# Kernel optimization log

Hardware: AMD Instinct MI355X
Metric: run time of the kernel (lower is better)

Reference implementation:

```python
import jax, jax.numpy as jnp
import numpy as np

N = 100000
IN_C = 128
OUT_C = 128
E = 1600000


def setup_inputs() -> dict:
    key = jax.random.key(0)
    k1, k2, k3, k4 = jax.random.split(key, 4)
    x = jax.random.normal(k1, (N, IN_C), dtype=jnp.float32)
    edge_index = jax.random.randint(k2, (2, E), 0, N, dtype=jnp.int64)
    # GCNConv params: linear weight (stored [in, out] for x @ W) and bias [out]
    W = jax.random.normal(k3, (IN_C, OUT_C), dtype=jnp.float32) / np.sqrt(IN_C)
    b = jax.random.normal(k4, (OUT_C,), dtype=jnp.float32) * 0.01
    return {"x": x, "edge_index": edge_index, "W": W, "b": b}


def reference(x, edge_index, W, b):
    n = x.shape[0]
    # add self loops (PyG GCNConv default add_self_loops=True)
    loop = jnp.arange(n, dtype=edge_index.dtype)
    src = jnp.concatenate([edge_index[0], loop])  # message sources
    dst = jnp.concatenate([edge_index[1], loop])  # aggregation targets
    # symmetric normalization: deg over targets (edge weight 1, incl. self loops)
    deg = jax.ops.segment_sum(jnp.ones_like(dst, dtype=x.dtype), dst, num_segments=n)
    dinv = jnp.where(deg > 0, jax.lax.rsqrt(deg), 0.0)
    norm = dinv[src] * dinv[dst]  # [E+N]
    # linear transform then gather-scale-scatter aggregation
    h = x @ W  # [N, out]
    msgs = h[src] * norm[:, None]  # [E+N, out] -- dominant memory traffic
    out = jax.ops.segment_sum(msgs, dst, num_segments=n)
    return out + b
```

## Files before the change

### kernel.cpp

```cpp
#include <hip/hip_runtime.h>


#define SCAN_T 256
#define SCAN_E 1024
#define WPB 4
#define CAP 1536
#define SC_T 8192

typedef __attribute__((ext_vector_type(8))) short short8;
typedef __attribute__((ext_vector_type(4))) float f32x4;

__device__ __forceinline__ unsigned short f2bf(float f) {
  unsigned int u = __float_as_uint(f);
  u += 0x7FFFu + ((u >> 16) & 1u);
  return (unsigned short)(u >> 16);
}
__device__ __forceinline__ float bf_lo(unsigned int u) { return __uint_as_float(u << 16); }
__device__ __forceinline__ float bf_hi(unsigned int u) { return __uint_as_float(u & 0xFFFF0000u); }


__global__ void k_zero(int* __restrict__ p, int m) {
  int i = blockIdx.x * blockDim.x + threadIdx.x;
  if (i < m) p[i] = 0;
}

__global__ void __launch_bounds__(512) k_scatter(
    const int* __restrict__ ei, int* __restrict__ bcursor,
    int* __restrict__ pairs, int E, int B) {
  __shared__ int hist[2048];
  int t = threadIdx.x;
  for (int b = t; b < B; b += 512) hist[b] = 0;
  __syncthreads();
  int e0 = blockIdx.x * SC_T;
  int eend = min(e0 + SC_T, E);
  for (int e = e0 + t * 4; e < eend; e += 2048) {
    if (e + 3 < eend) {
      int4 d = *(const int4*)(ei + E + e);
      atomicAdd(&hist[((unsigned)d.x) >> 6], 1);
      atomicAdd(&hist[((unsigned)d.y) >> 6], 1);
      atomicAdd(&hist[((unsigned)d.z) >> 6], 1);
      atomicAdd(&hist[((unsigned)d.w) >> 6], 1);
    } else {
      for (int q = e; q < eend; ++q) atomicAdd(&hist[((unsigned)ei[E + q]) >> 6], 1);
    }
  }
  __syncthreads();
  for (int b = t; b < B; b += 512) {
    int c = hist[b];
    hist[b] = c ? atomicAdd(&bcursor[b], c) : 0;
  }
  __syncthreads();
  for (int e = e0 + t * 4; e < eend; e += 2048) {
    if (e + 3 < eend) {
      int4 s = *(const int4*)(ei + e);
      int4 d = *(const int4*)(ei + E + e);
      int b0 = ((unsigned)d.x) >> 6; int p0 = atomicAdd(&hist[b0], 1);
      if (p0 < CAP) pairs[(size_t)b0 * CAP + p0] = ((d.x & 63) << 17) | s.x;
      int b1 = ((unsigned)d.y) >> 6; int p1 = atomicAdd(&hist[b1], 1);
      if (p1 < CAP) pairs[(size_t)b1 * CAP + p1] = ((d.y & 63) << 17) | s.y;
      int b2 = ((unsigned)d.z) >> 6; int p2 = atomicAdd(&hist[b2], 1);
      if (p2 < CAP) pairs[(size_t)b2 * CAP + p2] = ((d.z & 63) << 17) | s.z;
      int b3 = ((unsigned)d.w) >> 6; int p3 = atomicAdd(&hist[b3], 1);
      if (p3 < CAP) pairs[(size_t)b3 * CAP + p3] = ((d.w & 63) << 17) | s.w;
    } else {
      for (int q = e; q < eend; ++q) {
        int dst = ei[E + q], src = ei[q];
        int b0 = ((unsigned)dst) >> 6; int p0 = atomicAdd(&hist[b0], 1);
        if (p0 < CAP) pairs[(size_t)b0 * CAP + p0] = ((dst & 63) << 17) | src;
      }
    }
  }
}

__global__ void __launch_bounds__(256) k_sort_gemm(
    int* __restrict__ pairs, const int* __restrict__ bcursor,
    int* __restrict__ onc, float* __restrict__ dinv,
    const float* __restrict__ x, const float* __restrict__ W,
    unsigned short* __restrict__ h, int n) {
  __shared__ alignas(16) unsigned short Wt[128][136];
  __shared__ int pb[CAP];
  __shared__ int sorted[CAP];
  __shared__ int hist[64], base_[64], cur[64];
  __shared__ float dloc[64];
  int t = threadIdx.x;
  int b = blockIdx.x;
  if (t < 64) { hist[t] = 0; cur[t] = 0; }
  int cnt = min(bcursor[b], CAP);
  int* gp = pairs + (size_t)b * CAP;
  for (int i = t; i < cnt; i += 256) pb[i] = gp[i];
#pragma unroll
  for (int p = 0; p < 16; ++p) {
    int task = p * 256 + t;
    int kg = task >> 7, nn = task & 127;
    float w0 = W[(kg * 4 + 0) * 128 + nn];
    float w1 = W[(kg * 4 + 1) * 128 + nn];
    float w2 = W[(kg * 4 + 2) * 128 + nn];
    float w3 = W[(kg * 4 + 3) * 128 + nn];
    ushort4 u;
    u.x = f2bf(w0); u.y = f2bf(w1); u.z = f2bf(w2); u.w = f2bf(w3);
    *(ushort4*)&Wt[nn][kg * 4] = u;
  }
  __syncthreads();
  for (int i = t; i < cnt; i += 256) atomicAdd(&hist[pb[i] >> 17], 1);
  __syncthreads();
  if (t < 64) {
    int v = hist[t];
    int incl = v;
#pragma unroll
    for (int d = 1; d < 64; d <<= 1) {
      int u = __shfl_up(incl, d, 64);
      if (t >= d) incl += u;
    }
    base_[t] = incl - v;
    float di = rsqrtf((float)v + 1.0f);
    dloc[t] = di;
    int node = b * 64 + t;
    if (node < n) {
      onc[node] = ((incl - v) << 16) | v;
      dinv[node] = di;
    }
  }
  __syncthreads();
  for (int i = t; i < cnt; i += 256) {
    int p = pb[i];
    int d = p >> 17;
    int pos = base_[d] + atomicAdd(&cur[d], 1);
    sorted[pos] = p & 0x1FFFF;
  }
  __syncthreads();
  for (int i = t; i < cnt; i += 256) gp[i] = sorted[i];

  int w = t >> 6, lane = t & 63;
  int q = lane >> 4, m = lane & 15;
  int r0 = b * 64 + w * 16;
  f32x4 acc[8];
#pragma unroll
  for (int nt = 0; nt < 8; ++nt) acc[nt] = (f32x4){0.f, 0.f, 0.f, 0.f};
  float dscale[4];
#pragma unroll
  for (int rg = 0; rg < 4; ++rg) dscale[rg] = dloc[w * 16 + q * 4 + rg];
#pragma unroll
  for (int ks = 0; ks < 4; ++ks) {
    int row = r0 + m;
    row = row < n ? row : n - 1;
    const float* xp = x + (size_t)row * 128 + ks * 32 + q * 8;
    float4 a0 = *(const float4*)xp;
    float4 a1 = *(const float4*)(xp + 4);
    short8 af;
    af[0] = (short)f2bf(a0.x); af[1] = (short)f2bf(a0.y);
    af[2] = (short)f2bf(a0.z); af[3] = (short)f2bf(a0.w);
    af[4] = (short)f2bf(a1.x); af[5] = (short)f2bf(a1.y);
    af[6] = (short)f2bf(a1.z); af[7] = (short)f2bf(a1.w);
#pragma unroll
    for (int nt = 0; nt < 8; ++nt) {
      short8 bf = *(const short8*)&Wt[nt * 16 + m][ks * 32 + q * 8];
      acc[nt] = __builtin_amdgcn_mfma_f32_16x16x32_bf16(af, bf, acc[nt], 0, 0, 0);
    }
  }
#pragma unroll
  for (int nt = 0; nt < 8; ++nt)
#pragma unroll
    for (int rg = 0; rg < 4; ++rg) {
      int r = r0 + q * 4 + rg;
      if (r < n) h[(size_t)r * 128 + nt * 16 + m] = f2bf(acc[nt][rg] * dscale[rg]);
    }
}

__global__ void __launch_bounds__(256) k_agg_bias(
    const unsigned int* __restrict__ h2, const float* __restrict__ dinv,
    const int* __restrict__ onc, const int* __restrict__ pairs,
    const float* __restrict__ bias, float* __restrict__ out, int n) {
  int node = blockIdx.x * WPB + (threadIdx.x >> 6);
  int lane = threadIdx.x & 63;
  if (node >= n) return;
  unsigned int sp = h2[(size_t)node * 64 + lane];
  float ax = bf_lo(sp), ay = bf_hi(sp);
  int v = onc[node];
  int s = (node >> 6) * CAP + (v >> 16);
  int end = s + (v & 0xFFFF);
  const int* __restrict__ csr = pairs;
  for (; s + 8 <= end; s += 8) {
    int i0 = csr[s + 0], i1 = csr[s + 1], i2 = csr[s + 2], i3 = csr[s + 3];
    int i4 = csr[s + 4], i5 = csr[s + 5], i6 = csr[s + 6], i7 = csr[s + 7];
    unsigned int u0 = h2[(size_t)i0 * 64 + lane];
    unsigned int u1 = h2[(size_t)i1 * 64 + lane];
    unsigned int u2 = h2[(size_t)i2 * 64 + lane];
    unsigned int u3 = h2[(size_t)i3 * 64 + lane];
    unsigned int u4 = h2[(size_t)i4 * 64 + lane];
    unsigned int u5 = h2[(size_t)i5 * 64 + lane];
    unsigned int u6 = h2[(size_t)i6 * 64 + lane];
    unsigned int u7 = h2[(size_t)i7 * 64 + lane];
    ax += (bf_lo(u0) + bf_lo(u1)) + (bf_lo(u2) + bf_lo(u3)) +
          (bf_lo(u4) + bf_lo(u5)) + (bf_lo(u6) + bf_lo(u7));
    ay += (bf_hi(u0) + bf_hi(u1)) + (bf_hi(u2) + bf_hi(u3)) +
          (bf_hi(u4) + bf_hi(u5)) + (bf_hi(u6) + bf_hi(u7));
  }
  for (; s < end; ++s) {
    unsigned int u = h2[(size_t)csr[s] * 64 + lane];
    ax += bf_lo(u); ay += bf_hi(u);
  }
  float di = dinv[node];
  float2 bb = ((const float2*)bias)[lane];
  float2 r;
  r.x = fmaf(ax, di, bb.x);
  r.y = fmaf(ay, di, bb.y);
  ((float2*)out)[(size_t)node * 64 + lane] = r;
}


__global__ void k_init(int* __restrict__ cnt, int n) {
  int i = blockIdx.x * blockDim.x + threadIdx.x;
  if (i < n) cnt[i] = 0;
}

__global__ void k_count4(const int* __restrict__ ei, int* __restrict__ cnt, int E) {
  int i = blockIdx.x * blockDim.x + threadIdx.x;
  int e = i * 4;
  if (e + 3 < E) {
    int4 d = *(const int4*)(ei + E + e);
    atomicAdd(&cnt[d.x], 1); atomicAdd(&cnt[d.y], 1);
    atomicAdd(&cnt[d.z], 1); atomicAdd(&cnt[d.w], 1);
  } else {
    for (; e < E; ++e) atomicAdd(&cnt[ei[E + e]], 1);
  }
}

__global__ void k_scan_local(const int* __restrict__ cnt, int* __restrict__ offs,
                             int* __restrict__ bsums, int n) {
  __shared__ int sh[SCAN_T];
  int t = threadIdx.x;
  int base = blockIdx.x * SCAN_E + t * 4;
  int v0 = 0, v1 = 0, v2 = 0, v3 = 0;
  if (base + 0 < n) v0 = cnt[base + 0];
  if (base + 1 < n) v1 = cnt[base + 1];
  if (base + 2 < n) v2 = cnt[base + 2];
  if (base + 3 < n) v3 = cnt[base + 3];
  int sum = v0 + v1 + v2 + v3;
  sh[t] = sum;
  __syncthreads();
  for (int d = 1; d < SCAN_T; d <<= 1) {
    int xv = (t >= d) ? sh[t - d] : 0;
    __syncthreads();
    sh[t] += xv;
    __syncthreads();
  }
  int run = sh[t] - sum;
  if (base + 0 < n) offs[base + 0] = run; run += v0;
  if (base + 1 < n) offs[base + 1] = run; run += v1;
  if (base + 2 < n) offs[base + 2] = run; run += v2;
  if (base + 3 < n) offs[base + 3] = run;
  if (t == SCAN_T - 1) bsums[blockIdx.x] = sh[t];
}

__global__ void k_scan_bsums(int* __restrict__ bsums, int nb) {
  __shared__ int sh[SCAN_T];
  int t = threadIdx.x;
  int v = (t < nb) ? bsums[t] : 0;
  sh[t] = v;
  __syncthreads();
  for (int d = 1; d < SCAN_T; d <<= 1) {
    int xv = (t >= d) ? sh[t - d] : 0;
    __syncthreads();
    sh[t] += xv;
    __syncthreads();
  }
  if (t < nb) bsums[t] = sh[t] - v;
}

__global__ void k_scan_finish(int* __restrict__ offs, const int* __restrict__ bsums,
                              const int* __restrict__ cnt, int* __restrict__ offs2,
                              float* __restrict__ dinv, int n) {
  int i = blockIdx.x * blockDim.x + threadIdx.x;
  if (i < n) {
    int o = offs[i] + bsums[i / SCAN_E];
    offs[i] = o;
    offs2[i] = o;
    dinv[i] = rsqrtf((float)cnt[i] + 1.0f);
  }
}

__global__ void k_fill4(const int* __restrict__ ei, int* __restrict__ offs2,
                        int* __restrict__ csr, int E) {
  int i = blockIdx.x * blockDim.x + threadIdx.x;
  int e = i * 4;
  if (e + 3 < E) {
    int4 s = *(const int4*)(ei + e);
    int4 d = *(const int4*)(ei + E + e);
    csr[atomicAdd(&offs2[d.x], 1)] = s.x;
    csr[atomicAdd(&offs2[d.y], 1)] = s.y;
    csr[atomicAdd(&offs2[d.z], 1)] = s.z;
    csr[atomicAdd(&offs2[d.w], 1)] = s.w;
  } else {
    for (; e < E; ++e) csr[atomicAdd(&offs2[ei[E + e]], 1)] = ei[e];
  }
}

__global__ void __launch_bounds__(256) k_gemm_h(
    const float* __restrict__ x, const float* __restrict__ W,
    const float* __restrict__ dinv, unsigned short* __restrict__ h, int n) {
  __shared__ alignas(16) unsigned short Wt[128][136];
  int t = threadIdx.x;
#pragma unroll
  for (int p = 0; p < 16; ++p) {
    int task = p * 256 + t;
    int kg = task >> 7, nn = task & 127;
    float w0 = W[(kg * 4 + 0) * 128 + nn];
    float w1 = W[(kg * 4 + 1) * 128 + nn];
    float w2 = W[(kg * 4 + 2) * 128 + nn];
    float w3 = W[(kg * 4 + 3) * 128 + nn];
    ushort4 u;
    u.x = f2bf(w0); u.y = f2bf(w1); u.z = f2bf(w2); u.w = f2bf(w3);
    *(ushort4*)&Wt[nn][kg * 4] = u;
  }
  __syncthreads();
  int w = t >> 6, lane = t & 63;
  int q = lane >> 4, m = lane & 15;
  int r0 = blockIdx.x * 64 + w * 16;
  f32x4 acc[8];
#pragma unroll
  for (int nt = 0; nt < 8; ++nt) acc[nt] = (f32x4){0.f, 0.f, 0.f, 0.f};
  float dscale[4];
#pragma unroll
  for (int rg = 0; rg < 4; ++rg) {
    int r = r0 + q * 4 + rg;
    dscale[rg] = dinv[r < n ? r : n - 1];
  }
#pragma unroll
  for (int ks = 0; ks < 4; ++ks) {
    int row = r0 + m;
    row = row < n ? row : n - 1;
    const float* xp = x + (size_t)row * 128 + ks * 32 + q * 8;
    float4 a0 = *(const float4*)xp;
    float4 a1 = *(const float4*)(xp + 4);
    short8 af;
    af[0] = (short)f2bf(a0.x); af[1] = (short)f2bf(a0.y);
    af[2] = (short)f2bf(a0.z); af[3] = (short)f2bf(a0.w);
    af[4] = (short)f2bf(a1.x); af[5] = (short)f2bf(a1.y);
    af[6] = (short)f2bf(a1.z); af[7] = (short)f2bf(a1.w);
#pragma unroll
    for (int nt = 0; nt < 8; ++nt) {
      short8 bf = *(const short8*)&Wt[nt * 16 + m][ks * 32 + q * 8];
      acc[nt] = __builtin_amdgcn_mfma_f32_16x16x32_bf16(af, bf, acc[nt], 0, 0, 0);
    }
  }
#pragma unroll
  for (int nt = 0; nt < 8; ++nt)
#pragma unroll
    for (int rg = 0; rg < 4; ++rg) {
      int r = r0 + q * 4 + rg;
      if (r < n) h[(size_t)r * 128 + nt * 16 + m] = f2bf(acc[nt][rg] * dscale[rg]);
    }
}

__global__ void __launch_bounds__(256) k_agg_bias_csr(
    const unsigned int* __restrict__ h2, const float* __restrict__ dinv,
    const int* __restrict__ offs, const int* __restrict__ cnt,
    const int* __restrict__ csr, const float* __restrict__ bias,
    float* __restrict__ out, int n) {
  int node = blockIdx.x * WPB + (threadIdx.x >> 6);
  int lane = threadIdx.x & 63;
  if (node >= n) return;
  unsigned int sp = h2[(size_t)node * 64 + lane];
  float ax = bf_lo(sp), ay = bf_hi(sp);
  int s = offs[node];
  int end = s + cnt[node];
  for (; s + 8 <= end; s += 8) {
    int i0 = csr[s + 0], i1 = csr[s + 1], i2 = csr[s + 2], i3 = csr[s + 3];
    int i4 = csr[s + 4], i5 = csr[s + 5], i6 = csr[s + 6], i7 = csr[s + 7];
    unsigned int u0 = h2[(size_t)i0 * 64 + lane];
    unsigned int u1 = h2[(size_t)i1 * 64 + lane];
    unsigned int u2 = h2[(size_t)i2 * 64 + lane];
    unsigned int u3 = h2[(size_t)i3 * 64 + lane];
    unsigned int u4 = h2[(size_t)i4 * 64 + lane];
    unsigned int u5 = h2[(size_t)i5 * 64 + lane];
    unsigned int u6 = h2[(size_t)i6 * 64 + lane];
    unsigned int u7 = h2[(size_t)i7 * 64 + lane];
    ax += (bf_lo(u0) + bf_lo(u1)) + (bf_lo(u2) + bf_lo(u3)) +
          (bf_lo(u4) + bf_lo(u5)) + (bf_lo(u6) + bf_lo(u7));
    ay += (bf_hi(u0) + bf_hi(u1)) + (bf_hi(u2) + bf_hi(u3)) +
          (bf_hi(u4) + bf_hi(u5)) + (bf_hi(u6) + bf_hi(u7));
  }
  for (; s < end; ++s) {
    unsigned int u = h2[(size_t)csr[s] * 64 + lane];
    ax += bf_lo(u); ay += bf_hi(u);
  }
  float di = dinv[node];
  float2 bb = ((const float2*)bias)[lane];
  float2 r;
  r.x = fmaf(ax, di, bb.x);
  r.y = fmaf(ay, di, bb.y);
  ((float2*)out)[(size_t)node * 64 + lane] = r;
}

extern "C" void kernel_launch(void* const* d_in, const int* in_sizes, int n_in,
                              void* d_out, int out_size, void* d_ws, size_t ws_size,
                              hipStream_t stream) {
  const float* x = (const float*)d_in[0];
  const int* ei = (const int*)d_in[1];
  const float* Wm = (const float*)d_in[2];
  const float* bias = (const float*)d_in[3];
  float* out = (float*)d_out;

  int N = in_sizes[0] / 128;
  int E = in_sizes[1] / 2;
  int NB = (N + 63) >> 6;

  size_t need_new = (size_t)N * 8 + 8192 + (size_t)NB * CAP * 4 + (size_t)N * 256;

  if (ws_size >= need_new && N <= (1 << 17) && NB <= 2048) {
    char* p = (char*)d_ws;
    float* dinv = (float*)p;       p += (size_t)N * 4;
    int* onc = (int*)p;            p += (size_t)N * 4;
    int* bcursor = (int*)p;        p += 8192;
    int* pairs = (int*)p;          p += (size_t)NB * CAP * 4;
    unsigned short* h = (unsigned short*)p;

    k_zero<<<(NB + 255) / 256, 256, 0, stream>>>(bcursor, NB);
    k_scatter<<<(E + SC_T - 1) / SC_T, 512, 0, stream>>>(ei, bcursor, pairs, E, NB);
    k_sort_gemm<<<NB, 256, 0, stream>>>(pairs, bcursor, onc, dinv, x, Wm, h, N);
    k_agg_bias<<<(N + WPB - 1) / WPB, 256, 0, stream>>>(
        (const unsigned int*)h, dinv, onc, pairs, bias, out, N);
    return;
  }

  char* p = (char*)d_ws;
  int* cnt = (int*)p;        p += (size_t)N * 4;
  int* offs = (int*)p;       p += (size_t)N * 4;
  int* offs2 = (int*)p;      p += (size_t)N * 4;
  float* dinv = (float*)p;   p += (size_t)N * 4;
  int* bsums = (int*)p;      p += 1024;
  int* csr = (int*)p;        p += (size_t)E * 4;
  unsigned short* h = (unsigned short*)p;

  int nb_n = (N + 255) / 256;
  int nb_e4 = ((E + 3) / 4 + 255) / 256;
  int nb_scan = (N + SCAN_E - 1) / SCAN_E;

  k_init<<<nb_n, 256, 0, stream>>>(cnt, N);
  k_count4<<<nb_e4, 256, 0, stream>>>(ei, cnt, E);
  k_scan_local<<<nb_scan, SCAN_T, 0, stream>>>(cnt, offs, bsums, N);
  k_scan_bsums<<<1, SCAN_T, 0, stream>>>(bsums, nb_scan);
  k_scan_finish<<<nb_n, 256, 0, stream>>>(offs, bsums, cnt, offs2, dinv, N);
  k_fill4<<<nb_e4, 256, 0, stream>>>(ei, offs2, csr, E);
  k_gemm_h<<<(N + 63) / 64, 256, 0, stream>>>(x, Wm, dinv, h, N);
  k_agg_bias_csr<<<(N + WPB - 1) / WPB, 256, 0, stream>>>(
      (const unsigned int*)h, dinv, offs, cnt, csr, bias, out, N);
}
```

Baseline: 221.2 us.

## Overlap edge scatter with GEMM in one launch, split bucket sort out

The edge bucket-scatter and the dense x@W GEMM now share one launch: the first SB blocks scatter edges and the remaining blocks run the MFMA GEMM, so the two independent phases run concurrently. The per-bucket CSR sort and degree computation move to a separate kernel. Because the GEMM no longer has the degree, h is stored unscaled, and the aggregation kernel instead loads dinv[src] per edge and applies it with an FMA. This adds one small kernel launch and an extra gathered 4-byte load per edge in the memory-bound aggregation, in exchange for hiding the scatter behind the GEMM. The scatter tile size is halved to match 256-thread blocks.

```diff
diff --git a/kernel.cpp b/kernel.cpp
--- a/kernel.cpp
+++ b/kernel.cpp
@@ -5,7 +5,7 @@
 #define SCAN_E 1024
 #define WPB 4
 #define CAP 1536
-#define SC_T 8192
+#define SC_T 4096
 
 typedef __attribute__((ext_vector_type(8))) short short8;
 typedef __attribute__((ext_vector_type(4))) float f32x4;
@@ -24,70 +24,63 @@
   if (i < m) p[i] = 0;
 }
 
-__global__ void __launch_bounds__(512) k_scatter(
+__global__ void __launch_bounds__(256) k_scatter_gemm(
     const int* __restrict__ ei, int* __restrict__ bcursor,
-    int* __restrict__ pairs, int E, int B) {
-  __shared__ int hist[2048];
-  int t = threadIdx.x;
-  for (int b = t; b < B; b += 512) hist[b] = 0;
-  __syncthreads();
-  int e0 = blockIdx.x * SC_T;
-  int eend = min(e0 + SC_T, E);
-  for (int e = e0 + t * 4; e < eend; e += 2048) {
-    if (e + 3 < eend) {
-      int4 d = *(const int4*)(ei + E + e);
-      atomicAdd(&hist[((unsigned)d.x) >> 6], 1);
-      atomicAdd(&hist[((unsigned)d.y) >> 6], 1);
-      atomicAdd(&hist[((unsigned)d.z) >> 6], 1);
-      atomicAdd(&hist[((unsigned)d.w) >> 6], 1);
-    } else {
-      for (int q = e; q < eend; ++q) atomicAdd(&hist[((unsigned)ei[E + q]) >> 6], 1);
-    }
-  }
-  __syncthreads();
-  for (int b = t; b < B; b += 512) {
-    int c = hist[b];
-    hist[b] = c ? atomicAdd(&bcursor[b], c) : 0;
-  }
-  __syncthreads();
-  for (int e = e0 + t * 4; e < eend; e += 2048) {
-    if (e + 3 < eend) {
-      int4 s = *(const int4*)(ei + e);
-      int4 d = *(const int4*)(ei + E + e);
-      int b0 = ((unsigned)d.x) >> 6; int p0 = atomicAdd(&hist[b0], 1);
-      if (p0 < CAP) pairs[(size_t)b0 * CAP + p0] = ((d.x & 63) << 17) | s.x;
-      int b1 = ((unsigned)d.y) >> 6; int p1 = atomicAdd(&hist[b1], 1);
-      if (p1 < CAP) pairs[(size_t)b1 * CAP + p1] = ((d.y & 63) << 17) | s.y;
-      int b2 = ((unsigned)d.z) >> 6; int p2 = atomicAdd(&hist[b2], 1);
-      if (p2 < CAP) pairs[(size_t)b2 * CAP + p2] = ((d.z & 63) << 17) | s.z;
-      int b3 = ((unsigned)d.w) >> 6; int p3 = atomicAdd(&hist[b3], 1);
-      if (p3 < CAP) pairs[(size_t)b3 * CAP + p3] = ((d.w & 63) << 17) | s.w;
-    } else {
-      for (int q = e; q < eend; ++q) {
-        int dst = ei[E + q], src = ei[q];
-        int b0 = ((unsigned)dst) >> 6; int p0 = atomicAdd(&hist[b0], 1);
-        if (p0 < CAP) pairs[(size_t)b0 * CAP + p0] = ((dst & 63) << 17) | src;
-      }
-    }
-  }
-}
-
-__global__ void __launch_bounds__(256) k_sort_gemm(
-    int* __restrict__ pairs, const int* __restrict__ bcursor,
-    int* __restrict__ onc, float* __restrict__ dinv,
+    int* __restrict__ pairs, int E, int B, int SB,
     const float* __restrict__ x, const float* __restrict__ W,
     unsigned short* __restrict__ h, int n) {
-  __shared__ alignas(16) unsigned short Wt[128][136];
-  __shared__ int pb[CAP];
-  __shared__ int sorted[CAP];
-  __shared__ int hist[64], base_[64], cur[64];
-  __shared__ float dloc[64];
+  __shared__ alignas(16) char smem[128 * 136 * 2];
   int t = threadIdx.x;
-  int b = blockIdx.x;
-  if (t < 64) { hist[t] = 0; cur[t] = 0; }
-  int cnt = min(bcursor[b], CAP);
-  int* gp = pairs + (size_t)b * CAP;
-  for (int i = t; i < cnt; i += 256) pb[i] = gp[i];
+  int bid = blockIdx.x;
+
+  if (bid < SB) {
+    int* hist = (int*)smem;
+    for (int b = t; b < B; b += 256) hist[b] = 0;
+    __syncthreads();
+    int e0 = bid * SC_T;
+    int eend = min(e0 + SC_T, E);
+    for (int e = e0 + t * 4; e < eend; e += 1024) {
+      if (e + 3 < eend) {
+        int4 d = *(const int4*)(ei + E + e);
+        atomicAdd(&hist[((unsigned)d.x) >> 6], 1);
+        atomicAdd(&hist[((unsigned)d.y) >> 6], 1);
+        atomicAdd(&hist[((unsigned)d.z) >> 6], 1);
+        atomicAdd(&hist[((unsigned)d.w) >> 6], 1);
+      } else {
+        for (int q = e; q < eend; ++q) atomicAdd(&hist[((unsigned)ei[E + q]) >> 6], 1);
+      }
+    }
+    __syncthreads();
+    for (int b = t; b < B; b += 256) {
+      int c = hist[b];
+      hist[b] = c ? atomicAdd(&bcursor[b], c) : 0;
+    }
+    __syncthreads();
+    for (int e = e0 + t * 4; e < eend; e += 1024) {
+      if (e + 3 < eend) {
+        int4 s = *(const int4*)(ei + e);
+        int4 d = *(const int4*)(ei + E + e);
+        int b0 = ((unsigned)d.x) >> 6; int p0 = atomicAdd(&hist[b0], 1);
+        if (p0 < CAP) pairs[(size_t)b0 * CAP + p0] = ((d.x & 63) << 17) | s.x;
+        int b1 = ((unsigned)d.y) >> 6; int p1 = atomicAdd(&hist[b1], 1);
+        if (p1 < CAP) pairs[(size_t)b1 * CAP + p1] = ((d.y & 63) << 17) | s.y;
+        int b2 = ((unsigned)d.z) >> 6; int p2 = atomicAdd(&hist[b2], 1);
+        if (p2 < CAP) pairs[(size_t)b2 * CAP + p2] = ((d.z & 63) << 17) | s.z;
+        int b3 = ((unsigned)d.w) >> 6; int p3 = atomicAdd(&hist[b3], 1);
+        if (p3 < CAP) pairs[(size_t)b3 * CAP + p3] = ((d.w & 63) << 17) | s.w;
+      } else {
+        for (int q = e; q < eend; ++q) {
+          int dst = ei[E + q], src = ei[q];
+          int b0 = ((unsigned)dst) >> 6; int p0 = atomicAdd(&hist[b0], 1);
+          if (p0 < CAP) pairs[(size_t)b0 * CAP + p0] = ((dst & 63) << 17) | src;
+        }
+      }
+    }
+    return;
+  }
+
+  int b = bid - SB;
+  unsigned short (*Wt)[136] = (unsigned short (*)[136])smem;
 #pragma unroll
   for (int p = 0; p < 16; ++p) {
     int task = p * 256 + t;
@@ -101,44 +94,12 @@
     *(ushort4*)&Wt[nn][kg * 4] = u;
   }
   __syncthreads();
-  for (int i = t; i < cnt; i += 256) atomicAdd(&hist[pb[i] >> 17], 1);
-  __syncthreads();
-  if (t < 64) {
-    int v = hist[t];
-    int incl = v;
-#pragma unroll
-    for (int d = 1; d < 64; d <<= 1) {
-      int u = __shfl_up(incl, d, 64);
-      if (t >= d) incl += u;
-    }
-    base_[t] = incl - v;
-    float di = rsqrtf((float)v + 1.0f);
-    dloc[t] = di;
-    int node = b * 64 + t;
-    if (node < n) {
-      onc[node] = ((incl - v) << 16) | v;
-      dinv[node] = di;
-    }
-  }
-  __syncthreads();
-  for (int i = t; i < cnt; i += 256) {
-    int p = pb[i];
-    int d = p >> 17;
-    int pos = base_[d] + atomicAdd(&cur[d], 1);
-    sorted[pos] = p & 0x1FFFF;
-  }
-  __syncthreads();
-  for (int i = t; i < cnt; i += 256) gp[i] = sorted[i];
-
   int w = t >> 6, lane = t & 63;
   int q = lane >> 4, m = lane & 15;
   int r0 = b * 64 + w * 16;
   f32x4 acc[8];
 #pragma unroll
   for (int nt = 0; nt < 8; ++nt) acc[nt] = (f32x4){0.f, 0.f, 0.f, 0.f};
-  float dscale[4];
-#pragma unroll
-  for (int rg = 0; rg < 4; ++rg) dscale[rg] = dloc[w * 16 + q * 4 + rg];
 #pragma unroll
   for (int ks = 0; ks < 4; ++ks) {
     int row = r0 + m;
@@ -162,8 +123,49 @@
 #pragma unroll
     for (int rg = 0; rg < 4; ++rg) {
       int r = r0 + q * 4 + rg;
-      if (r < n) h[(size_t)r * 128 + nt * 16 + m] = f2bf(acc[nt][rg] * dscale[rg]);
-    }
+      if (r < n) h[(size_t)r * 128 + nt * 16 + m] = f2bf(acc[nt][rg]);
+    }
+}
+
+__global__ void __launch_bounds__(256) k_bucket_csr(
+    int* __restrict__ pairs, const int* __restrict__ bcursor,
+    int* __restrict__ onc, float* __restrict__ dinv, int n) {
+  __shared__ int pb[CAP];
+  __shared__ int sorted[CAP];
+  __shared__ int hist[64], base_[64], cur[64];
+  int t = threadIdx.x;
+  int b = blockIdx.x;
+  int cnt = min(bcursor[b], CAP);
+  int* gp = pairs + (size_t)b * CAP;
+  for (int i = t; i < cnt; i += 256) pb[i] = gp[i];
+  if (t < 64) { hist[t] = 0; cur[t] = 0; }
+  __syncthreads();
+  for (int i = t; i < cnt; i += 256) atomicAdd(&hist[pb[i] >> 17], 1);
+  __syncthreads();
+  if (t < 64) {
+    int v = hist[t];
+    int incl = v;
+#pragma unroll
+    for (int d = 1; d < 64; d <<= 1) {
+      int u = __shfl_up(incl, d, 64);
+      if (t >= d) incl += u;
+    }
+    base_[t] = incl - v;
+    int node = b * 64 + t;
+    if (node < n) {
+      onc[node] = ((incl - v) << 16) | v;
+      dinv[node] = rsqrtf((float)v + 1.0f);
+    }
+  }
+  __syncthreads();
+  for (int i = t; i < cnt; i += 256) {
+    int p = pb[i];
+    int d = p >> 17;
+    int pos = base_[d] + atomicAdd(&cur[d], 1);
+    sorted[pos] = p & 0x1FFFF;
+  }
+  __syncthreads();
+  for (int i = t; i < cnt; i += 256) gp[i] = sorted[i];
 }
 
 __global__ void __launch_bounds__(256) k_agg_bias(
@@ -173,8 +175,9 @@
   int node = blockIdx.x * WPB + (threadIdx.x >> 6);
   int lane = threadIdx.x & 63;
   if (node >= n) return;
+  float di = dinv[node];
   unsigned int sp = h2[(size_t)node * 64 + lane];
-  float ax = bf_lo(sp), ay = bf_hi(sp);
+  float ax = di * bf_lo(sp), ay = di * bf_hi(sp);
   int v = onc[node];
   int s = (node >> 6) * CAP + (v >> 16);
   int end = s + (v & 0xFFFF);
@@ -190,16 +193,23 @@
     unsigned int u5 = h2[(size_t)i5 * 64 + lane];
     unsigned int u6 = h2[(size_t)i6 * 64 + lane];
     unsigned int u7 = h2[(size_t)i7 * 64 + lane];
-    ax += (bf_lo(u0) + bf_lo(u1)) + (bf_lo(u2) + bf_lo(u3)) +
-          (bf_lo(u4) + bf_lo(u5)) + (bf_lo(u6) + bf_lo(u7));
-    ay += (bf_hi(u0) + bf_hi(u1)) + (bf_hi(u2) + bf_hi(u3)) +
-          (bf_hi(u4) + bf_hi(u5)) + (bf_hi(u6) + bf_hi(u7));
+    float d0 = dinv[i0], d1 = dinv[i1], d2 = dinv[i2], d3 = dinv[i3];
+    float d4 = dinv[i4], d5 = dinv[i5], d6 = dinv[i6], d7 = dinv[i7];
+    ax = fmaf(bf_lo(u0), d0, ax); ay = fmaf(bf_hi(u0), d0, ay);
+    ax = fmaf(bf_lo(u1), d1, ax); ay = fmaf(bf_hi(u1), d1, ay);
+    ax = fmaf(bf_lo(u2), d2, ax); ay = fmaf(bf_hi(u2), d2, ay);
+    ax = fmaf(bf_lo(u3), d3, ax); ay = fmaf(bf_hi(u3), d3, ay);
+    ax = fmaf(bf_lo(u4), d4, ax); ay = fmaf(bf_hi(u4), d4, ay);
+    ax = fmaf(bf_lo(u5), d5, ax); ay = fmaf(bf_hi(u5), d5, ay);
+    ax = fmaf(bf_lo(u6), d6, ax); ay = fmaf(bf_hi(u6), d6, ay);
+    ax = fmaf(bf_lo(u7), d7, ax); ay = fmaf(bf_hi(u7), d7, ay);
   }
   for (; s < end; ++s) {
-    unsigned int u = h2[(size_t)csr[s] * 64 + lane];
-    ax += bf_lo(u); ay += bf_hi(u);
-  }
-  float di = dinv[node];
+    int i0 = csr[s];
+    unsigned int u = h2[(size_t)i0 * 64 + lane];
+    float d0 = dinv[i0];
+    ax = fmaf(bf_lo(u), d0, ax); ay = fmaf(bf_hi(u), d0, ay);
+  }
   float2 bb = ((const float2*)bias)[lane];
   float2 r;
   r.x = fmaf(ax, di, bb.x);
@@ -404,6 +414,7 @@
   int N = in_sizes[0] / 128;
   int E = in_sizes[1] / 2;
   int NB = (N + 63) >> 6;
+  int SB = (E + SC_T - 1) / SC_T;
 
   size_t need_new = (size_t)N * 8 + 8192 + (size_t)NB * CAP * 4 + (size_t)N * 256;
 
@@ -416,8 +427,9 @@
     unsigned short* h = (unsigned short*)p;
 
     k_zero<<<(NB + 255) / 256, 256, 0, stream>>>(bcursor, NB);
-    k_scatter<<<(E + SC_T - 1) / SC_T, 512, 0, stream>>>(ei, bcursor, pairs, E, NB);
-    k_sort_gemm<<<NB, 256, 0, stream>>>(pairs, bcursor, onc, dinv, x, Wm, h, N);
+    k_scatter_gemm<<<SB + NB, 256, 0, stream>>>(ei, bcursor, pairs, E, NB, SB,
+                                                x, Wm, h, N);
+    k_bucket_csr<<<NB, 256, 0, stream>>>(pairs, bcursor, onc, dinv, N);
     k_agg_bias<<<(N + WPB - 1) / WPB, 256, 0, stream>>>(
         (const unsigned int*)h, dinv, onc, pairs, bias, out, N);
     return;
```

After: 225.3 us. No clear change (+1.9%).
